# Kernel optimization log

Measured on AMD Instinct MI355X. Metric: run time of the kernel, lower is better.

The kernel has to match this reference:

```python
import jax, jax.numpy as jnp
import numpy as np


def conv3x3(x, w, b):
    # stride 1, pad 1, NCHW / OIHW
    out = jax.lax.conv_general_dilated(x, w, (1, 1), ((1, 1), (1, 1)),
                                       dimension_numbers=('NCHW', 'OIHW', 'NCHW'))
    return out + b[None, :, None, None]


def bilinear_sample(x, ys, xs):
    # x: [B,C,H,W]; ys,xs: [B,K,H,W] float sampling coords.
    # mmcv-style: zero outside image, per-corner validity.
    B, C, H, W = x.shape
    x_flat = x.reshape(B, C, H * W)
    y0 = jnp.floor(ys)
    x0 = jnp.floor(xs)
    dy = ys - y0
    dx = xs - x0
    y0i = y0.astype(jnp.int32)
    x0i = x0.astype(jnp.int32)

    def corner(yc, xc, wgt):
        valid = (yc >= 0) & (yc < H) & (xc >= 0) & (xc < W)
        idx = jnp.clip(yc, 0, H - 1) * W + jnp.clip(xc, 0, W - 1)  # [B,K,H,W]
        idx_f = idx.reshape(B, -1)
        vals = jax.vmap(lambda xf, ix: xf[:, ix])(x_flat, idx_f)  # [B,C,K*H*W]
        vals = vals.reshape(B, C, *yc.shape[1:])
        return vals * (wgt * valid)[:, None]

    out = corner(y0i, x0i, (1 - dy) * (1 - dx))
    out = out + corner(y0i, x0i + 1, (1 - dy) * dx)
    out = out + corner(y0i + 1, x0i, dy * (1 - dx))
    out = out + corner(y0i + 1, x0i + 1, dy * dx)
    return out  # [B,C,K,H,W]


def avgpool3s2(z):
    # AvgPool2d(kernel=3, stride=2, padding=1), count_include_pad=True -> divide by 9
    s = jax.lax.reduce_window(z, 0.0, jax.lax.add, (1, 1, 3, 3), (1, 1, 2, 2),
                              ((0, 0), (0, 0), (1, 1), (1, 1)))
    return s / 9.0


def setup_inputs() -> dict:
    key = jax.random.key(0)
    k1, k2, k3 = jax.random.split(key, 3)
    C = 64
    x = jax.random.normal(k1, (4, C, 128, 128), dtype=jnp.float32)
    w_off = jax.random.normal(k2, (27, C, 3, 3), dtype=jnp.float32) * 0.02
    b_off = jnp.zeros((27,), dtype=jnp.float32)
    w_align = jax.random.normal(k3, (C, C, 3, 3), dtype=jnp.float32) * 0.02
    b_align = jnp.zeros((C,), dtype=jnp.float32)
    return {"x": x, "w_off": w_off, "b_off": b_off, "w_align": w_align, "b_align": b_align}


def reference(x, w_off, b_off, w_align, b_align):
    B, C, H, W = x.shape
    K = 9
    off_all = conv3x3(x, w_off, b_off)               # [B,27,H,W]
    offset = off_all[:, :2 * K]                      # [B,18,H,W]
    mask = 2.0 * jax.nn.sigmoid(off_all[:, 2 * K:])  # [B,9,H,W]
    off = offset.reshape(B, K, 2, H, W)
    dy = off[:, :, 0]
    dx = off[:, :, 1]
    # base kernel grid (dilation 1, pad 1): offsets in {-1,0,1}
    ky = (jnp.arange(K) // 3 - 1).astype(jnp.float32)
    kx = (jnp.arange(K) % 3 - 1).astype(jnp.float32)
    ys = jnp.arange(H, dtype=jnp.float32)[None, None, :, None] + ky[None, :, None, None] + dy
    xs = jnp.arange(W, dtype=jnp.float32)[None, None, None, :] + kx[None, :, None, None] + dx
    sampled = bilinear_sample(x, ys, xs) * mask[:, None]    # [B,C,K,H,W]
    w = jnp.einsum('bckhw,ock->bohw', sampled, w_align.reshape(C, C, K))
    w = w + b_align[None, :, None, None]
    w = jnp.exp(jax.nn.sigmoid(w))
    return avgpool3s2(w * x) / avgpool3s2(w)
```

## Files before the change

### kernel.cpp

```cpp
#include <hip/hip_runtime.h>
#include <hip/hip_bf16.h>

#define HW 16384
#define CC 64
#define BB 4

typedef __attribute__((ext_vector_type(8))) short bf8;
typedef __attribute__((ext_vector_type(4))) float f4;

static __device__ __forceinline__ float bf2f(unsigned short u) {
    return __uint_as_float(((unsigned)u) << 16);
}
static __device__ __forceinline__ unsigned short f2bf(float f) {
    __hip_bfloat16 h = __float2bfloat16(f);
    return *reinterpret_cast<unsigned short*>(&h);
}

__global__ __launch_bounds__(256) void k_prep_tx(const float* __restrict__ x,
                                                 const float* __restrict__ w_off,
                                                 const float* __restrict__ w_align,
                                                 unsigned short* __restrict__ xT,
                                                 unsigned short* __restrict__ wA,
                                                 unsigned short* __restrict__ Wal) {
    __shared__ unsigned T32[64 * 33];
    int bx = blockIdx.x, t = threadIdx.x;
    if (bx < 216) {
        int i = bx * 256 + t;
        if (i < 32 * 576) {
            int m = i / 576, r = i - m * 576, tt = r >> 6, c = r & 63;
            float v = (m < 27) ? w_off[m * 576 + c * 9 + tt] : 0.f;
            wA[i] = f2bf(v);
        } else {
            int j = i - 32 * 576;
            int o = j / 576, r = j - o * 576, tt = r >> 6, c = r & 63;
            Wal[j] = f2bf(w_align[o * 576 + c * 9 + tt]);
        }
        return;
    }
    int pix0 = (bx - 216) * 64;
    int b = pix0 >> 14, hw0 = pix0 & (HW - 1);
    const float* xb = x + (size_t)b * CC * HW + hw0;
#pragma unroll
    for (int u = 0; u < 8; u++) {
        int i = t + 256 * u;
        int cp = i >> 6, p = i & 63;
        float v0 = xb[(size_t)(2 * cp) * HW + p];
        float v1 = xb[(size_t)(2 * cp + 1) * HW + p];
        T32[p * 33 + cp] = (unsigned)f2bf(v0) | ((unsigned)f2bf(v1) << 16);
    }
    __syncthreads();
#pragma unroll
    for (int u = 0; u < 2; u++) {
        int i = t + 256 * u;
        int p = i >> 3, q = i & 7;
        uint4 qq;
        qq.x = T32[p * 33 + q * 4 + 0];
        qq.y = T32[p * 33 + q * 4 + 1];
        qq.z = T32[p * 33 + q * 4 + 2];
        qq.w = T32[p * 33 + q * 4 + 3];
        *(uint4*)(xT + ((size_t)b * HW + hw0 + p) * CC + q * 8) = qq;
    }
}

__global__ __launch_bounds__(256, 4) void k_conv(const unsigned short* __restrict__ xT,
                                                 const unsigned short* __restrict__ wA,
                                                 const float* __restrict__ b_off,
                                                 float* __restrict__ off) {
    __shared__ __align__(16) unsigned short WL[32 * 584];
    int t = threadIdx.x, lane = t & 63, wv = t >> 6;
    int quad = lane >> 4, col = lane & 15;
#pragma unroll
    for (int u = 0; u < 9; u++) {
        int idx = t + 256 * u;
        int row = idx / 72, jb = idx - row * 72;
        *(uint4*)(WL + row * 584 + jb * 8) = ((const uint4*)wA)[idx];
    }
    __syncthreads();

    int n = blockIdx.x * 64 + wv * 16 + col;
    int b = n >> 14, hw = n & (HW - 1), h = hw >> 7, w = hw & 127;
    const unsigned short* xTb = xT + (size_t)b * HW * CC;
    const bf8 zero = {0, 0, 0, 0, 0, 0, 0, 0};

    f4 acc0 = {0.f, 0.f, 0.f, 0.f};
    f4 acc1 = {0.f, 0.f, 0.f, 0.f};
#pragma unroll
    for (int tap = 0; tap < 9; tap++) {
        int dyt = tap / 3 - 1, dxt = tap - (tap / 3) * 3 - 1;
        int hs = h + dyt, ws = w + dxt;
        bool valid = ((unsigned)hs < 128u) && ((unsigned)ws < 128u);
        int hc = min(max(hs, 0), 127), wc = min(max(ws, 0), 127);
        const unsigned short* src = xTb + ((size_t)(hc * 128 + wc)) * CC + quad * 8;
        bf8 b0 = *(const bf8*)(src);
        bf8 b1 = *(const bf8*)(src + 32);
        b0 = valid ? b0 : zero;
        b1 = valid ? b1 : zero;
        const unsigned short* l0 = WL + col * 584 + tap * 64 + quad * 8;
        const unsigned short* l1 = WL + (col + 16) * 584 + tap * 64 + quad * 8;
        acc0 = __builtin_amdgcn_mfma_f32_16x16x32_bf16(*(const bf8*)l0, b0, acc0, 0, 0, 0);
        acc1 = __builtin_amdgcn_mfma_f32_16x16x32_bf16(*(const bf8*)l1, b0, acc1, 0, 0, 0);
        acc0 = __builtin_amdgcn_mfma_f32_16x16x32_bf16(*(const bf8*)(l0 + 32), b1, acc0, 0, 0, 0);
        acc1 = __builtin_amdgcn_mfma_f32_16x16x32_bf16(*(const bf8*)(l1 + 32), b1, acc1, 0, 0, 0);
    }
#pragma unroll
    for (int i = 0; i < 4; i++) {
        int o0 = quad * 4 + i;
        {
            float v = acc0[i] + b_off[o0];
            if (o0 >= 18) v = 2.f / (1.f + __expf(-v));
            off[((size_t)b * 27 + o0) * HW + hw] = v;
        }
        int o1 = 16 + o0;
        if (o1 < 27) {
            float v = acc1[i] + b_off[o1];
            if (o1 >= 18) v = 2.f / (1.f + __expf(-v));
            off[((size_t)b * 27 + o1) * HW + hw] = v;
        }
    }
}

__global__ __launch_bounds__(256, 3) void k_fused(const unsigned short* __restrict__ xT,
                                                  const float* __restrict__ off,
                                                  const unsigned short* __restrict__ Wal,
                                                  const float* __restrict__ b_align,
                                                  float* __restrict__ wten) {
    __shared__ __align__(16) unsigned short WB[2][64 * 200];

    int t = threadIdx.x, lane = t & 63, wv = t >> 6;
    int quad = lane >> 4, col = lane & 15;
    int pix0 = blockIdx.x * 64;
    int b = pix0 >> 14;
    int px = (pix0 & (HW - 1)) + wv * 16 + col;
    int h = px >> 7, w = px & 127;
    const unsigned short* xTb = xT + (size_t)b * HW * CC;
    const float* offp = off + (size_t)b * 27 * HW + px;

#pragma unroll
    for (int u = 0; u < 6; u++) {
        int idx = t + 256 * u;
        int row = idx / 24, jb = idx - row * 24;
        *(uint4*)(&WB[0][row * 200 + jb * 8]) = ((const uint4*)Wal)[row * 72 + jb];
    }
    __syncthreads();

    f4 acc[4];
#pragma unroll
    for (int mt = 0; mt < 4; mt++) acc[mt] = (f4){0.f, 0.f, 0.f, 0.f};

#pragma unroll
    for (int g = 0; g < 3; g++) {
        if (g < 2) {
#pragma unroll
            for (int u = 0; u < 6; u++) {
                int idx = t + 256 * u;
                int row = idx / 24, jb = idx - row * 24;
                *(uint4*)(&WB[(g + 1) & 1][row * 200 + jb * 8]) =
                    ((const uint4*)Wal)[row * 72 + (g + 1) * 24 + jb];
            }
        }
        const unsigned short* WLg = WB[g & 1];
#pragma unroll
        for (int kk = 0; kk < 3; kk++) {
            int k = 3 * g + kk;
            float dy = offp[(size_t)(2 * k) * HW];
            float dx = offp[(size_t)(2 * k + 1) * HW];
            float m  = offp[(size_t)(18 + k) * HW];
            int k3 = k / 3;
            float ys = (float)(h + k3 - 1) + dy;
            float xs = (float)(w + (k - 3 * k3) - 1) + dx;
            float y0f = floorf(ys), x0f = floorf(xs);
            float fy = ys - y0f, fx = xs - x0f;
            int y0 = (int)y0f, x0 = (int)x0f;
            int y1 = y0 + 1, x1 = x0 + 1;
            bool vy0 = (unsigned)y0 < 128u, vy1 = (unsigned)y1 < 128u;
            bool vx0 = (unsigned)x0 < 128u, vx1 = (unsigned)x1 < 128u;
            int cy0 = min(max(y0, 0), 127), cy1 = min(max(y1, 0), 127);
            int cx0 = min(max(x0, 0), 127), cx1 = min(max(x1, 0), 127);
            float w00 = (1.f - fy) * (1.f - fx) * ((vy0 && vx0) ? m : 0.f);
            float w01 = (1.f - fy) * fx         * ((vy0 && vx1) ? m : 0.f);
            float w10 = fy * (1.f - fx)         * ((vy1 && vx0) ? m : 0.f);
            float w11 = fy * fx                 * ((vy1 && vx1) ? m : 0.f);

            const unsigned short* c00 = xTb + ((size_t)(cy0 * 128 + cx0)) * CC + quad * 8;
            const unsigned short* c01 = xTb + ((size_t)(cy0 * 128 + cx1)) * CC + quad * 8;
            const unsigned short* c10 = xTb + ((size_t)(cy1 * 128 + cx0)) * CC + quad * 8;
            const unsigned short* c11 = xTb + ((size_t)(cy1 * 128 + cx1)) * CC + quad * 8;
            uint4 qa0 = *(const uint4*)(c00),      qa1 = *(const uint4*)(c01);
            uint4 qa2 = *(const uint4*)(c10),      qa3 = *(const uint4*)(c11);
            uint4 qb0 = *(const uint4*)(c00 + 32), qb1 = *(const uint4*)(c01 + 32);
            uint4 qb2 = *(const uint4*)(c10 + 32), qb3 = *(const uint4*)(c11 + 32);

            bf8 bfrag[2];
#pragma unroll
            for (int h2 = 0; h2 < 2; h2++) {
                const unsigned short* u00 = (const unsigned short*)(h2 ? &qb0 : &qa0);
                const unsigned short* u01 = (const unsigned short*)(h2 ? &qb1 : &qa1);
                const unsigned short* u10 = (const unsigned short*)(h2 ? &qb2 : &qa2);
                const unsigned short* u11 = (const unsigned short*)(h2 ? &qb3 : &qa3);
                unsigned short ov[8];
#pragma unroll
                for (int j = 0; j < 8; j++) {
                    float v = w00 * bf2f(u00[j]) + w01 * bf2f(u01[j])
                            + w10 * bf2f(u10[j]) + w11 * bf2f(u11[j]);
                    ov[j] = f2bf(v);
                }
                bfrag[h2] = *(const bf8*)ov;
            }
#pragma unroll
            for (int h2 = 0; h2 < 2; h2++) {
#pragma unroll
                for (int mt = 0; mt < 4; mt++) {
                    const bf8 a = *(const bf8*)(WLg + (size_t)(mt * 16 + col) * 200
                                                + kk * 64 + h2 * 32 + quad * 8);
                    acc[mt] = __builtin_amdgcn_mfma_f32_16x16x32_bf16(a, bfrag[h2], acc[mt], 0, 0, 0);
                }
            }
        }
        if (g < 2) __syncthreads();
    }

    float* wb = wten + (size_t)b * CC * HW + px;
#pragma unroll
    for (int mt = 0; mt < 4; mt++)
#pragma unroll
        for (int i = 0; i < 4; i++) {
            int o = mt * 16 + quad * 4 + i;
            float u = acc[mt][i] + b_align[o];
            float sg = 1.f / (1.f + __expf(-u));
            wb[(size_t)o * HW] = __expf(sg);
        }
}

__global__ __launch_bounds__(256) void k_pool(const float* __restrict__ x,
                                              const float* __restrict__ wten,
                                              float* __restrict__ out) {
    int idx = blockIdx.x * 256 + threadIdx.x;
    int ow = idx & 63;
    int oh = (idx >> 6) & 63;
    int bc = idx >> 12;
    const float* wp = wten + (size_t)bc * HW;
    const float* xp = x + (size_t)bc * HW;
    float num = 0.f, den = 0.f;
#pragma unroll
    for (int iy = 0; iy < 3; iy++) {
        int y = 2 * oh + iy - 1;
        if ((unsigned)y >= 128u) continue;
#pragma unroll
        for (int ix = 0; ix < 3; ix++) {
            int xc = 2 * ow + ix - 1;
            if ((unsigned)xc >= 128u) continue;
            float wv = wp[y * 128 + xc];
            float xv = xp[y * 128 + xc];
            num = fmaf(wv, xv, num);
            den += wv;
        }
    }
    out[idx] = num / den;
}

extern "C" void kernel_launch(void* const* d_in, const int* in_sizes, int n_in,
                              void* d_out, int out_size, void* d_ws, size_t ws_size,
                              hipStream_t stream) {
    const float* x       = (const float*)d_in[0];
    const float* w_off   = (const float*)d_in[1];
    const float* b_off   = (const float*)d_in[2];
    const float* w_align = (const float*)d_in[3];
    const float* b_align = (const float*)d_in[4];
    float* out = (float*)d_out;

    char* p = (char*)d_ws;
    float* off  = (float*)p;                  p += (size_t)BB * 27 * HW * 4;
    float* wten = (float*)p;                  p += (size_t)BB * CC * HW * 4;
    unsigned short* xT  = (unsigned short*)p; p += (size_t)BB * HW * CC * 2;
    unsigned short* wA  = (unsigned short*)p; p += 32 * 576 * 2;
    unsigned short* Wal = (unsigned short*)p;

    k_prep_tx<<<dim3(1240), dim3(256), 0, stream>>>(x, w_off, w_align, xT, wA, Wal);
    k_conv<<<dim3(1024), dim3(256), 0, stream>>>(xT, wA, b_off, off);
    k_fused<<<dim3(1024), dim3(256), 0, stream>>>(xT, off, Wal, b_align, wten);
    k_pool<<<dim3(4096), dim3(256), 0, stream>>>(x, wten, out);
}
```

Before: 135.6 us.

## Split fused deformable sample+GEMM into separate sampling and GEMM kernels

Replaces the fused kernel, which bilinearly sampled x and fed the result straight into MFMA, with two kernels. The first writes a bf16 sampled matrix S of shape pixels x 576 to workspace, launched over 9 kernel taps. The second runs a GEMM over S with weights held in LDS, split into two 32-channel output halves. This aims for better occupancy and memory-level parallelism in the gather, at the cost of a roughly 75 MB round trip through global memory for S. Each S row is also read twice, once per output half.

```diff
diff --git a/kernel.cpp b/kernel.cpp
--- a/kernel.cpp
+++ b/kernel.cpp
@@ -119,116 +119,115 @@
     }
 }
 
-__global__ __launch_bounds__(256, 3) void k_fused(const unsigned short* __restrict__ xT,
-                                                  const float* __restrict__ off,
-                                                  const unsigned short* __restrict__ Wal,
-                                                  const float* __restrict__ b_align,
-                                                  float* __restrict__ wten) {
-    __shared__ __align__(16) unsigned short WB[2][64 * 200];
-
+__global__ __launch_bounds__(256, 8) void k_sample(const unsigned short* __restrict__ xT,
+                                                   const float* __restrict__ off,
+                                                   unsigned short* __restrict__ S) {
+    int t = threadIdx.x;
+    int k = blockIdx.y;
+    int pxl = t >> 2, cq = t & 3;
+    int pg = blockIdx.x * 64 + pxl;
+    int b = pg >> 14, hw = pg & (HW - 1), h = hw >> 7, w = hw & 127;
+    const unsigned short* xTb = xT + (size_t)b * HW * CC;
+    const float* offb = off + (size_t)b * 27 * HW + hw;
+
+    float dy = offb[(size_t)(2 * k) * HW];
+    float dx = offb[(size_t)(2 * k + 1) * HW];
+    float m  = offb[(size_t)(18 + k) * HW];
+    int k3 = k / 3;
+    float ys = (float)(h + k3 - 1) + dy;
+    float xs = (float)(w + (k - 3 * k3) - 1) + dx;
+    float y0f = floorf(ys), x0f = floorf(xs);
+    float fy = ys - y0f, fx = xs - x0f;
+    int y0 = (int)y0f, x0 = (int)x0f;
+    int y1 = y0 + 1, x1 = x0 + 1;
+    bool vy0 = (unsigned)y0 < 128u, vy1 = (unsigned)y1 < 128u;
+    bool vx0 = (unsigned)x0 < 128u, vx1 = (unsigned)x1 < 128u;
+    int cy0 = min(max(y0, 0), 127), cy1 = min(max(y1, 0), 127);
+    int cx0 = min(max(x0, 0), 127), cx1 = min(max(x1, 0), 127);
+    float w00 = (1.f - fy) * (1.f - fx) * ((vy0 && vx0) ? m : 0.f);
+    float w01 = (1.f - fy) * fx         * ((vy0 && vx1) ? m : 0.f);
+    float w10 = fy * (1.f - fx)         * ((vy1 && vx0) ? m : 0.f);
+    float w11 = fy * fx                 * ((vy1 && vx1) ? m : 0.f);
+
+    const unsigned short* c00 = xTb + ((size_t)(cy0 * 128 + cx0)) * CC + cq * 16;
+    const unsigned short* c01 = xTb + ((size_t)(cy0 * 128 + cx1)) * CC + cq * 16;
+    const unsigned short* c10 = xTb + ((size_t)(cy1 * 128 + cx0)) * CC + cq * 16;
+    const unsigned short* c11 = xTb + ((size_t)(cy1 * 128 + cx1)) * CC + cq * 16;
+    uint4 qa0 = *(const uint4*)(c00),     qa1 = *(const uint4*)(c01);
+    uint4 qa2 = *(const uint4*)(c10),     qa3 = *(const uint4*)(c11);
+    uint4 qb0 = *(const uint4*)(c00 + 8), qb1 = *(const uint4*)(c01 + 8);
+    uint4 qb2 = *(const uint4*)(c10 + 8), qb3 = *(const uint4*)(c11 + 8);
+
+    unsigned short* dst = S + (size_t)pg * 576 + k * 64 + cq * 16;
+#pragma unroll
+    for (int h2 = 0; h2 < 2; h2++) {
+        const unsigned short* u00 = (const unsigned short*)(h2 ? &qb0 : &qa0);
+        const unsigned short* u01 = (const unsigned short*)(h2 ? &qb1 : &qa1);
+        const unsigned short* u10 = (const unsigned short*)(h2 ? &qb2 : &qa2);
+        const unsigned short* u11 = (const unsigned short*)(h2 ? &qb3 : &qa3);
+        unsigned short ov[8];
+#pragma unroll
+        for (int j = 0; j < 8; j++) {
+            float v = w00 * bf2f(u00[j]) + w01 * bf2f(u01[j])
+                    + w10 * bf2f(u10[j]) + w11 * bf2f(u11[j]);
+            ov[j] = f2bf(v);
+        }
+        uint4 qq;
+        qq.x = ov[0] | ((unsigned)ov[1] << 16);
+        qq.y = ov[2] | ((unsigned)ov[3] << 16);
+        qq.z = ov[4] | ((unsigned)ov[5] << 16);
+        qq.w = ov[6] | ((unsigned)ov[7] << 16);
+        *(uint4*)(dst + h2 * 8) = qq;
+    }
+}
+
+__global__ __launch_bounds__(256, 4) void k_gemm(const unsigned short* __restrict__ S,
+                                                 const unsigned short* __restrict__ Wal,
+                                                 const float* __restrict__ b_align,
+                                                 float* __restrict__ wten) {
+    __shared__ __align__(16) uint4 WL4[32 * 72];
     int t = threadIdx.x, lane = t & 63, wv = t >> 6;
     int quad = lane >> 4, col = lane & 15;
-    int pix0 = blockIdx.x * 64;
-    int b = pix0 >> 14;
-    int px = (pix0 & (HW - 1)) + wv * 16 + col;
-    int h = px >> 7, w = px & 127;
-    const unsigned short* xTb = xT + (size_t)b * HW * CC;
-    const float* offp = off + (size_t)b * 27 * HW + px;
-
-#pragma unroll
-    for (int u = 0; u < 6; u++) {
-        int idx = t + 256 * u;
-        int row = idx / 24, jb = idx - row * 24;
-        *(uint4*)(&WB[0][row * 200 + jb * 8]) = ((const uint4*)Wal)[row * 72 + jb];
+    int half = blockIdx.y;
+    const uint4* Wal4 = (const uint4*)Wal;
+#pragma unroll
+    for (int u = 0; u < 9; u++) {
+        int f = t + 256 * u;
+        WL4[f] = Wal4[(half * 32 + (f & 31)) * 72 + (f >> 5)];
     }
     __syncthreads();
 
-    f4 acc[4];
-#pragma unroll
-    for (int mt = 0; mt < 4; mt++) acc[mt] = (f4){0.f, 0.f, 0.f, 0.f};
-
-#pragma unroll
-    for (int g = 0; g < 3; g++) {
-        if (g < 2) {
-#pragma unroll
-            for (int u = 0; u < 6; u++) {
-                int idx = t + 256 * u;
-                int row = idx / 24, jb = idx - row * 24;
-                *(uint4*)(&WB[(g + 1) & 1][row * 200 + jb * 8]) =
-                    ((const uint4*)Wal)[row * 72 + (g + 1) * 24 + jb];
-            }
-        }
-        const unsigned short* WLg = WB[g & 1];
-#pragma unroll
-        for (int kk = 0; kk < 3; kk++) {
-            int k = 3 * g + kk;
-            float dy = offp[(size_t)(2 * k) * HW];
-            float dx = offp[(size_t)(2 * k + 1) * HW];
-            float m  = offp[(size_t)(18 + k) * HW];
-            int k3 = k / 3;
-            float ys = (float)(h + k3 - 1) + dy;
-            float xs = (float)(w + (k - 3 * k3) - 1) + dx;
-            float y0f = floorf(ys), x0f = floorf(xs);
-            float fy = ys - y0f, fx = xs - x0f;
-            int y0 = (int)y0f, x0 = (int)x0f;
-            int y1 = y0 + 1, x1 = x0 + 1;
-            bool vy0 = (unsigned)y0 < 128u, vy1 = (unsigned)y1 < 128u;
-            bool vx0 = (unsigned)x0 < 128u, vx1 = (unsigned)x1 < 128u;
-            int cy0 = min(max(y0, 0), 127), cy1 = min(max(y1, 0), 127);
-            int cx0 = min(max(x0, 0), 127), cx1 = min(max(x1, 0), 127);
-            float w00 = (1.f - fy) * (1.f - fx) * ((vy0 && vx0) ? m : 0.f);
-            float w01 = (1.f - fy) * fx         * ((vy0 && vx1) ? m : 0.f);
-            float w10 = fy * (1.f - fx)         * ((vy1 && vx0) ? m : 0.f);
-            float w11 = fy * fx                 * ((vy1 && vx1) ? m : 0.f);
-
-            const unsigned short* c00 = xTb + ((size_t)(cy0 * 128 + cx0)) * CC + quad * 8;
-            const unsigned short* c01 = xTb + ((size_t)(cy0 * 128 + cx1)) * CC + quad * 8;
-            const unsigned short* c10 = xTb + ((size_t)(cy1 * 128 + cx0)) * CC + quad * 8;
-            const unsigned short* c11 = xTb + ((size_t)(cy1 * 128 + cx1)) * CC + quad * 8;
-            uint4 qa0 = *(const uint4*)(c00),      qa1 = *(const uint4*)(c01);
-            uint4 qa2 = *(const uint4*)(c10),      qa3 = *(const uint4*)(c11);
-            uint4 qb0 = *(const uint4*)(c00 + 32), qb1 = *(const uint4*)(c01 + 32);
-            uint4 qb2 = *(const uint4*)(c10 + 32), qb3 = *(const uint4*)(c11 + 32);
-
-            bf8 bfrag[2];
-#pragma unroll
-            for (int h2 = 0; h2 < 2; h2++) {
-                const unsigned short* u00 = (const unsigned short*)(h2 ? &qb0 : &qa0);
-                const unsigned short* u01 = (const unsigned short*)(h2 ? &qb1 : &qa1);
-                const unsigned short* u10 = (const unsigned short*)(h2 ? &qb2 : &qa2);
-                const unsigned short* u11 = (const unsigned short*)(h2 ? &qb3 : &qa3);
-                unsigned short ov[8];
-#pragma unroll
-                for (int j = 0; j < 8; j++) {
-                    float v = w00 * bf2f(u00[j]) + w01 * bf2f(u01[j])
-                            + w10 * bf2f(u10[j]) + w11 * bf2f(u11[j]);
-                    ov[j] = f2bf(v);
-                }
-                bfrag[h2] = *(const bf8*)ov;
-            }
-#pragma unroll
-            for (int h2 = 0; h2 < 2; h2++) {
-#pragma unroll
-                for (int mt = 0; mt < 4; mt++) {
-                    const bf8 a = *(const bf8*)(WLg + (size_t)(mt * 16 + col) * 200
-                                                + kk * 64 + h2 * 32 + quad * 8);
-                    acc[mt] = __builtin_amdgcn_mfma_f32_16x16x32_bf16(a, bfrag[h2], acc[mt], 0, 0, 0);
-                }
-            }
-        }
-        if (g < 2) __syncthreads();
-    }
-
-    float* wb = wten + (size_t)b * CC * HW + px;
-#pragma unroll
-    for (int mt = 0; mt < 4; mt++)
-#pragma unroll
-        for (int i = 0; i < 4; i++) {
-            int o = mt * 16 + quad * 4 + i;
-            float u = acc[mt][i] + b_align[o];
+    int pg = blockIdx.x * 64 + wv * 16 + col;
+    int b = pg >> 14, hw = pg & (HW - 1);
+    const unsigned short* srow = S + (size_t)pg * 576 + quad * 8;
+
+    f4 acc0 = {0.f, 0.f, 0.f, 0.f};
+    f4 acc1 = {0.f, 0.f, 0.f, 0.f};
+#pragma unroll
+    for (int s = 0; s < 18; s++) {
+        bf8 bfrag = *(const bf8*)(srow + s * 32);
+        bf8 a0 = *(const bf8*)&WL4[col + 32 * (s * 4 + quad)];
+        bf8 a1 = *(const bf8*)&WL4[16 + col + 32 * (s * 4 + quad)];
+        acc0 = __builtin_amdgcn_mfma_f32_16x16x32_bf16(a0, bfrag, acc0, 0, 0, 0);
+        acc1 = __builtin_amdgcn_mfma_f32_16x16x32_bf16(a1, bfrag, acc1, 0, 0, 0);
+    }
+    int ob = half * 32;
+    float* wb = wten + (size_t)b * CC * HW + hw;
+#pragma unroll
+    for (int i = 0; i < 4; i++) {
+        {
+            int o = ob + quad * 4 + i;
+            float u = acc0[i] + b_align[o];
             float sg = 1.f / (1.f + __expf(-u));
             wb[(size_t)o * HW] = __expf(sg);
         }
+        {
+            int o = ob + 16 + quad * 4 + i;
+            float u = acc1[i] + b_align[o];
+            float sg = 1.f / (1.f + __expf(-u));
+            wb[(size_t)o * HW] = __expf(sg);
+        }
+    }
 }
 
 __global__ __launch_bounds__(256) void k_pool(const float* __restrict__ x,
@@ -273,10 +272,12 @@
     float* wten = (float*)p;                  p += (size_t)BB * CC * HW * 4;
     unsigned short* xT  = (unsigned short*)p; p += (size_t)BB * HW * CC * 2;
     unsigned short* wA  = (unsigned short*)p; p += 32 * 576 * 2;
-    unsigned short* Wal = (unsigned short*)p;
+    unsigned short* Wal = (unsigned short*)p; p += 64 * 576 * 2;
+    unsigned short* S   = (unsigned short*)p;
 
     k_prep_tx<<<dim3(1240), dim3(256), 0, stream>>>(x, w_off, w_align, xT, wA, Wal);
     k_conv<<<dim3(1024), dim3(256), 0, stream>>>(xT, wA, b_off, off);
-    k_fused<<<dim3(1024), dim3(256), 0, stream>>>(xT, off, Wal, b_align, wten);
+    k_sample<<<dim3(1024, 9), dim3(256), 0, stream>>>(xT, off, S);
+    k_gemm<<<dim3(1024, 2), dim3(256), 0, stream>>>(S, Wal, b_align, wten);
     k_pool<<<dim3(4096), dim3(256), 0, stream>>>(x, wten, out);
 }
```

New measurement: 148.3 us. +9.4%, slower.

## Pre-swizzle align weights into MFMA fragment order and drop LDS staging

Applied to the files above, without the earlier changes.

The prep kernel now writes the align-conv weights in a layout where each lane's 8-element MFMA A-fragment is contiguous per (tap, half, row, quad). The fused kernel uses single-wave 64-thread blocks (4096 of them) that read these fragments straight from global/L2 instead of staging weights through double-buffered shared memory with barriers. This removes LDS usage and block syncs to raise occupancy, at the cost of every wave re-reading the full weight set from cache.

```diff
diff --git a/kernel.cpp b/kernel.cpp
--- a/kernel.cpp
+++ b/kernel.cpp
@@ -21,7 +21,7 @@
                                                  const float* __restrict__ w_align,
                                                  unsigned short* __restrict__ xT,
                                                  unsigned short* __restrict__ wA,
-                                                 unsigned short* __restrict__ Wal) {
+                                                 unsigned short* __restrict__ W2) {
     __shared__ unsigned T32[64 * 33];
     int bx = blockIdx.x, t = threadIdx.x;
     if (bx < 216) {
@@ -32,8 +32,12 @@
             wA[i] = f2bf(v);
         } else {
             int j = i - 32 * 576;
-            int o = j / 576, r = j - o * 576, tt = r >> 6, c = r & 63;
-            Wal[j] = f2bf(w_align[o * 576 + c * 9 + tt]);
+            int f = j >> 3, jj = j & 7;
+            int s = f >> 8, rem = f & 255;
+            int row = rem >> 2, quad = rem & 3;
+            int c = ((s & 1) << 5) + quad * 8 + jj;
+            int tt = s >> 1;
+            W2[j] = f2bf(w_align[row * 576 + c * 9 + tt]);
         }
         return;
     }
@@ -119,104 +123,79 @@
     }
 }
 
-__global__ __launch_bounds__(256, 3) void k_fused(const unsigned short* __restrict__ xT,
-                                                  const float* __restrict__ off,
-                                                  const unsigned short* __restrict__ Wal,
-                                                  const float* __restrict__ b_align,
-                                                  float* __restrict__ wten) {
-    __shared__ __align__(16) unsigned short WB[2][64 * 200];
-
-    int t = threadIdx.x, lane = t & 63, wv = t >> 6;
+__global__ __launch_bounds__(64, 4) void k_fused(const unsigned short* __restrict__ xT,
+                                                 const float* __restrict__ off,
+                                                 const unsigned short* __restrict__ W2,
+                                                 const float* __restrict__ b_align,
+                                                 float* __restrict__ wten) {
+    int lane = threadIdx.x;
     int quad = lane >> 4, col = lane & 15;
-    int pix0 = blockIdx.x * 64;
+    int pix0 = blockIdx.x * 16;
     int b = pix0 >> 14;
-    int px = (pix0 & (HW - 1)) + wv * 16 + col;
+    int px = (pix0 & (HW - 1)) + col;
     int h = px >> 7, w = px & 127;
     const unsigned short* xTb = xT + (size_t)b * HW * CC;
     const float* offp = off + (size_t)b * 27 * HW + px;
 
-#pragma unroll
-    for (int u = 0; u < 6; u++) {
-        int idx = t + 256 * u;
-        int row = idx / 24, jb = idx - row * 24;
-        *(uint4*)(&WB[0][row * 200 + jb * 8]) = ((const uint4*)Wal)[row * 72 + jb];
-    }
-    __syncthreads();
-
     f4 acc[4];
 #pragma unroll
     for (int mt = 0; mt < 4; mt++) acc[mt] = (f4){0.f, 0.f, 0.f, 0.f};
 
 #pragma unroll
-    for (int g = 0; g < 3; g++) {
-        if (g < 2) {
-#pragma unroll
-            for (int u = 0; u < 6; u++) {
-                int idx = t + 256 * u;
-                int row = idx / 24, jb = idx - row * 24;
-                *(uint4*)(&WB[(g + 1) & 1][row * 200 + jb * 8]) =
-                    ((const uint4*)Wal)[row * 72 + (g + 1) * 24 + jb];
+    for (int k = 0; k < 9; k++) {
+        float dy = offp[(size_t)(2 * k) * HW];
+        float dx = offp[(size_t)(2 * k + 1) * HW];
+        float m  = offp[(size_t)(18 + k) * HW];
+        int k3 = k / 3;
+        float ys = (float)(h + k3 - 1) + dy;
+        float xs = (float)(w + (k - 3 * k3) - 1) + dx;
+        float y0f = floorf(ys), x0f = floorf(xs);
+        float fy = ys - y0f, fx = xs - x0f;
+        int y0 = (int)y0f, x0 = (int)x0f;
+        int y1 = y0 + 1, x1 = x0 + 1;
+        bool vy0 = (unsigned)y0 < 128u, vy1 = (unsigned)y1 < 128u;
+        bool vx0 = (unsigned)x0 < 128u, vx1 = (unsigned)x1 < 128u;
+        int cy0 = min(max(y0, 0), 127), cy1 = min(max(y1, 0), 127);
+        int cx0 = min(max(x0, 0), 127), cx1 = min(max(x1, 0), 127);
+        float w00 = (1.f - fy) * (1.f - fx) * ((vy0 && vx0) ? m : 0.f);
+        float w01 = (1.f - fy) * fx         * ((vy0 && vx1) ? m : 0.f);
+        float w10 = fy * (1.f - fx)         * ((vy1 && vx0) ? m : 0.f);
+        float w11 = fy * fx                 * ((vy1 && vx1) ? m : 0.f);
+
+        const unsigned short* c00 = xTb + ((size_t)(cy0 * 128 + cx0)) * CC + quad * 8;
+        const unsigned short* c01 = xTb + ((size_t)(cy0 * 128 + cx1)) * CC + quad * 8;
+        const unsigned short* c10 = xTb + ((size_t)(cy1 * 128 + cx0)) * CC + quad * 8;
+        const unsigned short* c11 = xTb + ((size_t)(cy1 * 128 + cx1)) * CC + quad * 8;
+        uint4 qa0 = *(const uint4*)(c00),      qa1 = *(const uint4*)(c01);
+        uint4 qa2 = *(const uint4*)(c10),      qa3 = *(const uint4*)(c11);
+        uint4 qb0 = *(const uint4*)(c00 + 32), qb1 = *(const uint4*)(c01 + 32);
+        uint4 qb2 = *(const uint4*)(c10 + 32), qb3 = *(const uint4*)(c11 + 32);
+
+        bf8 bfrag[2];
+#pragma unroll
+        for (int h2 = 0; h2 < 2; h2++) {
+            const unsigned short* u00 = (const unsigned short*)(h2 ? &qb0 : &qa0);
+            const unsigned short* u01 = (const unsigned short*)(h2 ? &qb1 : &qa1);
+            const unsigned short* u10 = (const unsigned short*)(h2 ? &qb2 : &qa2);
+            const unsigned short* u11 = (const unsigned short*)(h2 ? &qb3 : &qa3);
+            unsigned short ov[8];
+#pragma unroll
+            for (int j = 0; j < 8; j++) {
+                float v = w00 * bf2f(u00[j]) + w01 * bf2f(u01[j])
+                        + w10 * bf2f(u10[j]) + w11 * bf2f(u11[j]);
+                ov[j] = f2bf(v);
             }
-        }
-        const unsigned short* WLg = WB[g & 1];
-#pragma unroll
-        for (int kk = 0; kk < 3; kk++) {
-            int k = 3 * g + kk;
-            float dy = offp[(size_t)(2 * k) * HW];
-            float dx = offp[(size_t)(2 * k + 1) * HW];
-            float m  = offp[(size_t)(18 + k) * HW];
-            int k3 = k / 3;
-            float ys = (float)(h + k3 - 1) + dy;
-            float xs = (float)(w + (k - 3 * k3) - 1) + dx;
-            float y0f = floorf(ys), x0f = floorf(xs);
-            float fy = ys - y0f, fx = xs - x0f;
-            int y0 = (int)y0f, x0 = (int)x0f;
-            int y1 = y0 + 1, x1 = x0 + 1;
-            bool vy0 = (unsigned)y0 < 128u, vy1 = (unsigned)y1 < 128u;
-            bool vx0 = (unsigned)x0 < 128u, vx1 = (unsigned)x1 < 128u;
-            int cy0 = min(max(y0, 0), 127), cy1 = min(max(y1, 0), 127);
-            int cx0 = min(max(x0, 0), 127), cx1 = min(max(x1, 0), 127);
-            float w00 = (1.f - fy) * (1.f - fx) * ((vy0 && vx0) ? m : 0.f);
-            float w01 = (1.f - fy) * fx         * ((vy0 && vx1) ? m : 0.f);
-            float w10 = fy * (1.f - fx)         * ((vy1 && vx0) ? m : 0.f);
-            float w11 = fy * fx                 * ((vy1 && vx1) ? m : 0.f);
-
-            const unsigned short* c00 = xTb + ((size_t)(cy0 * 128 + cx0)) * CC + quad * 8;
-            const unsigned short* c01 = xTb + ((size_t)(cy0 * 128 + cx1)) * CC + quad * 8;
-            const unsigned short* c10 = xTb + ((size_t)(cy1 * 128 + cx0)) * CC + quad * 8;
-            const unsigned short* c11 = xTb + ((size_t)(cy1 * 128 + cx1)) * CC + quad * 8;
-            uint4 qa0 = *(const uint4*)(c00),      qa1 = *(const uint4*)(c01);
-            uint4 qa2 = *(const uint4*)(c10),      qa3 = *(const uint4*)(c11);
-            uint4 qb0 = *(const uint4*)(c00 + 32), qb1 = *(const uint4*)(c01 + 32);
-            uint4 qb2 = *(const uint4*)(c10 + 32), qb3 = *(const uint4*)(c11 + 32);
-
-            bf8 bfrag[2];
-#pragma unroll
-            for (int h2 = 0; h2 < 2; h2++) {
-                const unsigned short* u00 = (const unsigned short*)(h2 ? &qb0 : &qa0);
-                const unsigned short* u01 = (const unsigned short*)(h2 ? &qb1 : &qa1);
-                const unsigned short* u10 = (const unsigned short*)(h2 ? &qb2 : &qa2);
-                const unsigned short* u11 = (const unsigned short*)(h2 ? &qb3 : &qa3);
-                unsigned short ov[8];
-#pragma unroll
-                for (int j = 0; j < 8; j++) {
-                    float v = w00 * bf2f(u00[j]) + w01 * bf2f(u01[j])
-                            + w10 * bf2f(u10[j]) + w11 * bf2f(u11[j]);
-                    ov[j] = f2bf(v);
-                }
-                bfrag[h2] = *(const bf8*)ov;
+            bfrag[h2] = *(const bf8*)ov;
+        }
+#pragma unroll
+        for (int h2 = 0; h2 < 2; h2++) {
+            int s = 2 * k + h2;
+#pragma unroll
+            for (int mt = 0; mt < 4; mt++) {
+                bf8 a = *(const bf8*)(W2 + ((size_t)(s * 256 + (mt * 16 + col) * 4 + quad)) * 8);
+                acc[mt] = __builtin_amdgcn_mfma_f32_16x16x32_bf16(a, bfrag[h2], acc[mt], 0, 0, 0);
             }
-#pragma unroll
-            for (int h2 = 0; h2 < 2; h2++) {
-#pragma unroll
-                for (int mt = 0; mt < 4; mt++) {
-                    const bf8 a = *(const bf8*)(WLg + (size_t)(mt * 16 + col) * 200
-                                                + kk * 64 + h2 * 32 + quad * 8);
-                    acc[mt] = __builtin_amdgcn_mfma_f32_16x16x32_bf16(a, bfrag[h2], acc[mt], 0, 0, 0);
-                }
-            }
-        }
-        if (g < 2) __syncthreads();
+        }
     }
 
     float* wb = wten + (size_t)b * CC * HW + px;
@@ -273,10 +252,10 @@
     float* wten = (float*)p;                  p += (size_t)BB * CC * HW * 4;
     unsigned short* xT  = (unsigned short*)p; p += (size_t)BB * HW * CC * 2;
     unsigned short* wA  = (unsigned short*)p; p += 32 * 576 * 2;
-    unsigned short* Wal = (unsigned short*)p;
-
-    k_prep_tx<<<dim3(1240), dim3(256), 0, stream>>>(x, w_off, w_align, xT, wA, Wal);
+    unsigned short* W2  = (unsigned short*)p;
+
+    k_prep_tx<<<dim3(1240), dim3(256), 0, stream>>>(x, w_off, w_align, xT, wA, W2);
     k_conv<<<dim3(1024), dim3(256), 0, stream>>>(xT, wA, b_off, off);
-    k_fused<<<dim3(1024), dim3(256), 0, stream>>>(xT, off, Wal, b_align, wten);
+    k_fused<<<dim3(4096), dim3(64), 0, stream>>>(xT, off, W2, b_align, wten);
     k_pool<<<dim3(4096), dim3(256), 0, stream>>>(x, wten, out);
 }
```

Measured after the change: 143.1 us. 5.5% more time.

## Merge offset conv into deformable sampling kernel and remap blocks for XCD locality

Applied to the files above, without the earlier changes.

The offset/mask convolution is fused into the deformable-sampling GEMM kernel, so offsets stay in shared memory and the off tensor never makes a global round trip. The conv weights are pre-swizzled into an MFMA fragment layout and read directly from global instead of being staged in LDS. Block indices in the prep, merged and pool kernels are permuted so neighbouring tiles land on the same XCD, aiming for better L2 reuse. In exchange, the Wal weight staging loses its double buffer and gains an extra barrier per group, and the merged kernel's higher register and LDS use may lower occupancy.

```diff
diff --git a/kernel.cpp b/kernel.cpp
--- a/kernel.cpp
+++ b/kernel.cpp
@@ -20,24 +20,27 @@
                                                  const float* __restrict__ w_off,
                                                  const float* __restrict__ w_align,
                                                  unsigned short* __restrict__ xT,
-                                                 unsigned short* __restrict__ wA,
+                                                 unsigned short* __restrict__ wC2,
                                                  unsigned short* __restrict__ Wal) {
     __shared__ unsigned T32[64 * 33];
     int bx = blockIdx.x, t = threadIdx.x;
     if (bx < 216) {
         int i = bx * 256 + t;
-        if (i < 32 * 576) {
-            int m = i / 576, r = i - m * 576, tt = r >> 6, c = r & 63;
-            float v = (m < 27) ? w_off[m * 576 + c * 9 + tt] : 0.f;
-            wA[i] = f2bf(v);
+        if (i < 18432) {
+            int j = i & 7, quad = (i >> 3) & 3, row = (i >> 5) & 31, s = i >> 10;
+            int c = ((s & 1) << 5) + quad * 8 + j, tt = s >> 1;
+            float v = (row < 27) ? w_off[row * 576 + c * 9 + tt] : 0.f;
+            wC2[i] = f2bf(v);
         } else {
-            int j = i - 32 * 576;
-            int o = j / 576, r = j - o * 576, tt = r >> 6, c = r & 63;
-            Wal[j] = f2bf(w_align[o * 576 + c * 9 + tt]);
+            int j2 = i - 18432;
+            int o = j2 / 576, r = j2 - o * 576, tt = r >> 6, c = r & 63;
+            Wal[j2] = f2bf(w_align[o * 576 + c * 9 + tt]);
         }
         return;
     }
-    int pix0 = (bx - 216) * 64;
+    int local = bx - 216;
+    int vb = (local & 7) * 128 + (local >> 3);
+    int pix0 = vb * 64;
     int b = pix0 >> 14, hw0 = pix0 & (HW - 1);
     const float* xb = x + (size_t)b * CC * HW + hw0;
 #pragma unroll
@@ -62,28 +65,29 @@
     }
 }
 
-__global__ __launch_bounds__(256, 4) void k_conv(const unsigned short* __restrict__ xT,
-                                                 const unsigned short* __restrict__ wA,
-                                                 const float* __restrict__ b_off,
-                                                 float* __restrict__ off) {
-    __shared__ __align__(16) unsigned short WL[32 * 584];
+__global__ __launch_bounds__(256) void k_merged(const unsigned short* __restrict__ xT,
+                                                const unsigned short* __restrict__ wC2,
+                                                const unsigned short* __restrict__ Wal,
+                                                const float* __restrict__ b_off,
+                                                const float* __restrict__ b_align,
+                                                float* __restrict__ wten) {
+    __shared__ __align__(16) unsigned short WB[64 * 200];
+    __shared__ float offL[27][64];
+
     int t = threadIdx.x, lane = t & 63, wv = t >> 6;
     int quad = lane >> 4, col = lane & 15;
-#pragma unroll
-    for (int u = 0; u < 9; u++) {
-        int idx = t + 256 * u;
-        int row = idx / 72, jb = idx - row * 72;
-        *(uint4*)(WL + row * 584 + jb * 8) = ((const uint4*)wA)[idx];
-    }
-    __syncthreads();
-
-    int n = blockIdx.x * 64 + wv * 16 + col;
-    int b = n >> 14, hw = n & (HW - 1), h = hw >> 7, w = hw & 127;
+    int bxr = blockIdx.x;
+    int bx = (bxr & 7) * 128 + (bxr >> 3);
+    int pix0 = bx * 64;
+    int b = pix0 >> 14;
+    int pl = wv * 16 + col;
+    int px = (pix0 & (HW - 1)) + pl;
+    int h = px >> 7, w = px & 127;
     const unsigned short* xTb = xT + (size_t)b * HW * CC;
     const bf8 zero = {0, 0, 0, 0, 0, 0, 0, 0};
 
-    f4 acc0 = {0.f, 0.f, 0.f, 0.f};
-    f4 acc1 = {0.f, 0.f, 0.f, 0.f};
+    f4 c0 = {0.f, 0.f, 0.f, 0.f};
+    f4 c1 = {0.f, 0.f, 0.f, 0.f};
 #pragma unroll
     for (int tap = 0; tap < 9; tap++) {
         int dyt = tap / 3 - 1, dxt = tap - (tap / 3) * 3 - 1;
@@ -95,51 +99,26 @@
         bf8 b1 = *(const bf8*)(src + 32);
         b0 = valid ? b0 : zero;
         b1 = valid ? b1 : zero;
-        const unsigned short* l0 = WL + col * 584 + tap * 64 + quad * 8;
-        const unsigned short* l1 = WL + (col + 16) * 584 + tap * 64 + quad * 8;
-        acc0 = __builtin_amdgcn_mfma_f32_16x16x32_bf16(*(const bf8*)l0, b0, acc0, 0, 0, 0);
-        acc1 = __builtin_amdgcn_mfma_f32_16x16x32_bf16(*(const bf8*)l1, b0, acc1, 0, 0, 0);
-        acc0 = __builtin_amdgcn_mfma_f32_16x16x32_bf16(*(const bf8*)(l0 + 32), b1, acc0, 0, 0, 0);
-        acc1 = __builtin_amdgcn_mfma_f32_16x16x32_bf16(*(const bf8*)(l1 + 32), b1, acc1, 0, 0, 0);
+#pragma unroll
+        for (int h2 = 0; h2 < 2; h2++) {
+            int s = 2 * tap + h2;
+            bf8 bb = h2 ? b1 : b0;
+            const bf8 a0 = *(const bf8*)(wC2 + (size_t)s * 1024 + col * 32 + quad * 8);
+            const bf8 a1 = *(const bf8*)(wC2 + (size_t)s * 1024 + 512 + col * 32 + quad * 8);
+            c0 = __builtin_amdgcn_mfma_f32_16x16x32_bf16(a0, bb, c0, 0, 0, 0);
+            c1 = __builtin_amdgcn_mfma_f32_16x16x32_bf16(a1, bb, c1, 0, 0, 0);
+        }
     }
 #pragma unroll
     for (int i = 0; i < 4; i++) {
         int o0 = quad * 4 + i;
-        {
-            float v = acc0[i] + b_off[o0];
-            if (o0 >= 18) v = 2.f / (1.f + __expf(-v));
-            off[((size_t)b * 27 + o0) * HW + hw] = v;
-        }
+        offL[o0][pl] = c0[i] + b_off[o0];
         int o1 = 16 + o0;
         if (o1 < 27) {
-            float v = acc1[i] + b_off[o1];
+            float v = c1[i] + b_off[o1];
             if (o1 >= 18) v = 2.f / (1.f + __expf(-v));
-            off[((size_t)b * 27 + o1) * HW + hw] = v;
-        }
-    }
-}
-
-__global__ __launch_bounds__(256, 3) void k_fused(const unsigned short* __restrict__ xT,
-                                                  const float* __restrict__ off,
-                                                  const unsigned short* __restrict__ Wal,
-                                                  const float* __restrict__ b_align,
-                                                  float* __restrict__ wten) {
-    __shared__ __align__(16) unsigned short WB[2][64 * 200];
-
-    int t = threadIdx.x, lane = t & 63, wv = t >> 6;
-    int quad = lane >> 4, col = lane & 15;
-    int pix0 = blockIdx.x * 64;
-    int b = pix0 >> 14;
-    int px = (pix0 & (HW - 1)) + wv * 16 + col;
-    int h = px >> 7, w = px & 127;
-    const unsigned short* xTb = xT + (size_t)b * HW * CC;
-    const float* offp = off + (size_t)b * 27 * HW + px;
-
-#pragma unroll
-    for (int u = 0; u < 6; u++) {
-        int idx = t + 256 * u;
-        int row = idx / 24, jb = idx - row * 24;
-        *(uint4*)(&WB[0][row * 200 + jb * 8]) = ((const uint4*)Wal)[row * 72 + jb];
+            offL[o1][pl] = v;
+        }
     }
     __syncthreads();
 
@@ -149,22 +128,20 @@
 
 #pragma unroll
     for (int g = 0; g < 3; g++) {
-        if (g < 2) {
-#pragma unroll
-            for (int u = 0; u < 6; u++) {
-                int idx = t + 256 * u;
-                int row = idx / 24, jb = idx - row * 24;
-                *(uint4*)(&WB[(g + 1) & 1][row * 200 + jb * 8]) =
-                    ((const uint4*)Wal)[row * 72 + (g + 1) * 24 + jb];
-            }
-        }
-        const unsigned short* WLg = WB[g & 1];
+#pragma unroll
+        for (int u = 0; u < 6; u++) {
+            int idx = t + 256 * u;
+            int row = idx / 24, jb = idx - row * 24;
+            *(uint4*)(&WB[row * 200 + jb * 8]) = ((const uint4*)Wal)[row * 72 + g * 24 + jb];
+        }
+        __syncthreads();
+
 #pragma unroll
         for (int kk = 0; kk < 3; kk++) {
             int k = 3 * g + kk;
-            float dy = offp[(size_t)(2 * k) * HW];
-            float dx = offp[(size_t)(2 * k + 1) * HW];
-            float m  = offp[(size_t)(18 + k) * HW];
+            float dy = offL[2 * k][pl];
+            float dx = offL[2 * k + 1][pl];
+            float m  = offL[18 + k][pl];
             int k3 = k / 3;
             float ys = (float)(h + k3 - 1) + dy;
             float xs = (float)(w + (k - 3 * k3) - 1) + dx;
@@ -210,8 +187,8 @@
             for (int h2 = 0; h2 < 2; h2++) {
 #pragma unroll
                 for (int mt = 0; mt < 4; mt++) {
-                    const bf8 a = *(const bf8*)(WLg + (size_t)(mt * 16 + col) * 200
-                                                + kk * 64 + h2 * 32 + quad * 8);
+                    const bf8 a = *(const bf8*)(&WB[(size_t)(mt * 16 + col) * 200
+                                                + kk * 64 + h2 * 32 + quad * 8]);
                     acc[mt] = __builtin_amdgcn_mfma_f32_16x16x32_bf16(a, bfrag[h2], acc[mt], 0, 0, 0);
                 }
             }
@@ -234,7 +211,12 @@
 __global__ __launch_bounds__(256) void k_pool(const float* __restrict__ x,
                                               const float* __restrict__ wten,
                                               float* __restrict__ out) {
-    int idx = blockIdx.x * 256 + threadIdx.x;
+    int d = blockIdx.x;
+    int xg = d & 7, i = d >> 3;
+    int b = xg >> 1, sub_hi = xg & 1;
+    int c = i >> 3, sub_lo = i & 7;
+    int vb = ((b * 64 + c) * 16) + sub_hi * 8 + sub_lo;
+    int idx = vb * 256 + threadIdx.x;
     int ow = idx & 63;
     int oh = (idx >> 6) & 63;
     int bc = idx >> 12;
@@ -269,14 +251,12 @@
     float* out = (float*)d_out;
 
     char* p = (char*)d_ws;
-    float* off  = (float*)p;                  p += (size_t)BB * 27 * HW * 4;
     float* wten = (float*)p;                  p += (size_t)BB * CC * HW * 4;
     unsigned short* xT  = (unsigned short*)p; p += (size_t)BB * HW * CC * 2;
-    unsigned short* wA  = (unsigned short*)p; p += 32 * 576 * 2;
+    unsigned short* wC2 = (unsigned short*)p; p += 18432 * 2;
     unsigned short* Wal = (unsigned short*)p;
 
-    k_prep_tx<<<dim3(1240), dim3(256), 0, stream>>>(x, w_off, w_align, xT, wA, Wal);
-    k_conv<<<dim3(1024), dim3(256), 0, stream>>>(xT, wA, b_off, off);
-    k_fused<<<dim3(1024), dim3(256), 0, stream>>>(xT, off, Wal, b_align, wten);
+    k_prep_tx<<<dim3(1240), dim3(256), 0, stream>>>(x, w_off, w_align, xT, wC2, Wal);
+    k_merged<<<dim3(1024), dim3(256), 0, stream>>>(xT, wC2, Wal, b_off, b_align, wten);
     k_pool<<<dim3(4096), dim3(256), 0, stream>>>(x, wten, out);
 }
```

New measurement: 137.3 us. About the same (+1.3%).
